# Kernel optimization log

Measured on AMD Instinct MI355X. Metric: run time of the kernel, lower is better.

## Reference

```python
import jax, jax.numpy as jnp
import numpy as np

N_ATOMS = 100000; E_ATOMS = 200000; N_AMINO = 10240; E_AMINO = 20480; B = 512
D_IN = 40; D_E = 11; H1 = 20; H2 = 20; H3 = 20; D_AA = 8; H_ARMA = 128; K = 3; T = 7
F1 = 256; F2 = 128; F3 = 64


def setup_inputs() -> dict:
    key = jax.random.key(0)
    ks = jax.random.split(key, 40)
    s = 0.05
    inp = {}
    inp['x'] = jax.random.normal(ks[0], (N_ATOMS, D_IN), dtype=jnp.float32)
    inp['edge_index'] = jax.random.randint(ks[1], (2, E_ATOMS), 0, N_ATOMS, dtype=jnp.int32)
    inp['edge_attr'] = jax.random.normal(ks[2], (E_ATOMS, D_E), dtype=jnp.float32)
    inp['monomer_labels'] = jax.random.randint(ks[3], (N_ATOMS,), 0, N_AMINO, dtype=jnp.int32)
    inp['aminoacids_features'] = jax.random.normal(ks[4], (N_AMINO, D_AA), dtype=jnp.float32)
    inp['amino_edge_index'] = jax.random.randint(ks[5], (2, E_AMINO), 0, N_AMINO, dtype=jnp.int32)
    inp['amino_batch'] = jnp.sort(jax.random.randint(ks[6], (N_AMINO,), 0, B, dtype=jnp.int32))
    # NNConv params: edge-MLP (Linear(D_E, in*out)), root weight, bias
    inp['nn1_w'] = jax.random.normal(ks[7], (D_E, D_IN * H1)) * s
    inp['nn1_b'] = jax.random.normal(ks[8], (D_IN * H1,)) * s
    inp['root1'] = jax.random.normal(ks[9], (D_IN, H1)) * s
    inp['b1'] = jax.random.normal(ks[10], (H1,)) * s
    inp['nn2_w'] = jax.random.normal(ks[11], (D_E, H1 * H2)) * s
    inp['nn2_b'] = jax.random.normal(ks[12], (H1 * H2,)) * s
    inp['root2'] = jax.random.normal(ks[13], (H1, H2)) * s
    inp['b2'] = jax.random.normal(ks[14], (H2,)) * s
    inp['nn3_w'] = jax.random.normal(ks[15], (D_E, H2 * H3)) * s
    inp['nn3_b'] = jax.random.normal(ks[16], (H2 * H3,)) * s
    inp['root3'] = jax.random.normal(ks[17], (H2, H3)) * s
    inp['b3'] = jax.random.normal(ks[18], (H3,)) * s
    # ARMAConv params (K stacks, T layers, shared_weights=False)
    F_ARMA_IN = H3 + D_AA
    inp['arma_init'] = jax.random.normal(ks[19], (K, F_ARMA_IN, H_ARMA)) * s
    inp['arma_w'] = jax.random.normal(ks[20], (T - 1, K, H_ARMA, H_ARMA)) * s
    inp['arma_root'] = jax.random.normal(ks[21], (T, K, F_ARMA_IN, H_ARMA)) * s
    inp['arma_bias'] = jax.random.normal(ks[22], (T, K, 1, H_ARMA)) * s
    # FCN head
    inp['l1_w'] = jax.random.normal(ks[23], (H_ARMA, F1)) * s
    inp['l1_b'] = jax.random.normal(ks[24], (F1,)) * s
    inp['l2_w'] = jax.random.normal(ks[25], (F1, F2)) * s
    inp['l2_b'] = jax.random.normal(ks[26], (F2,)) * s
    inp['l3_w'] = jax.random.normal(ks[27], (F2, F3)) * s
    inp['l3_b'] = jax.random.normal(ks[28], (F3,)) * s
    inp['l4_w'] = jax.random.normal(ks[29], (F3, 1)) * s
    inp['l4_b'] = jax.random.normal(ks[30], (1,)) * s
    return inp


def _nnconv(x, ei, ea, w_nn, b_nn, root, bias, out_dim):
    # PyG NNConv (aggr='add'): out_i = x_i @ root + sum_{j->i} x_j @ W(e_ji) + bias
    E, d_in = ea.shape[0], x.shape[1]
    W = (ea @ w_nn + b_nn).reshape(E, d_in, out_dim)  # per-edge weight matrices
    msg = jnp.einsum('ei,eio->eo', x[ei[0]], W)       # gather + batched matvec
    agg = jax.ops.segment_sum(msg, ei[1], num_segments=x.shape[0])
    return x @ root + agg + bias


def _arma(x, ei, init_w, w, root_w, bias):
    # PyG ARMAConv: sym-normalized adjacency (no self loops), K stacks, T layers, ReLU act
    N = x.shape[0]
    deg = jax.ops.segment_sum(jnp.ones(ei.shape[1], x.dtype), ei[1], num_segments=N)
    dinv = jnp.where(deg > 0, deg ** -0.5, 0.0)
    norm = dinv[ei[0]] * dinv[ei[1]]  # [E_amino]
    out = None
    for t in range(T):
        h = jnp.einsum('nf,kfo->kno', x, init_w) if t == 0 else jnp.einsum('knf,kfo->kno', out, w[t - 1])
        msg = h[:, ei[0], :] * norm[None, :, None]
        h = jax.vmap(lambda m: jax.ops.segment_sum(m, ei[1], num_segments=N))(msg)
        h = h + jnp.einsum('nf,kfo->kno', x, root_w[t]) + bias[t]
        out = jax.nn.relu(h)
    return out.mean(0)  # mean over stacks


def reference(x, edge_index, edge_attr, monomer_labels, aminoacids_features,
              amino_edge_index, amino_batch,
              nn1_w, nn1_b, root1, b1, nn2_w, nn2_b, root2, b2, nn3_w, nn3_b, root3, b3,
              arma_init, arma_w, arma_root, arma_bias,
              l1_w, l1_b, l2_w, l2_b, l3_w, l3_b, l4_w, l4_b):
    h = jax.nn.relu(_nnconv(x, edge_index, edge_attr, nn1_w, nn1_b, root1, b1, H1))
    h = jax.nn.relu(_nnconv(h, edge_index, edge_attr, nn2_w, nn2_b, root2, b2, H2))
    h = jax.nn.relu(_nnconv(h, edge_index, edge_attr, nn3_w, nn3_b, root3, b3, H3))
    # per-graph loop flattened: atoms -> amino-acid sum readout (graphs disjoint)
    aa = jax.ops.segment_sum(h, monomer_labels, num_segments=N_AMINO)
    aa = jnp.concatenate([aa, aminoacids_features], axis=1)  # [N_AMINO, H3+8]
    aa = jax.nn.relu(_arma(aa, amino_edge_index, arma_init, arma_w, arma_root, arma_bias))
    g = jax.ops.segment_sum(aa, amino_batch, num_segments=B)  # per-graph sum readout
    p = jax.nn.relu(g @ l1_w + l1_b)  # dropout is identity in eval mode
    p = jax.nn.relu(p @ l2_w + l2_b)
    p = jax.nn.relu(p @ l3_w + l3_b)
    return (p @ l4_w + l4_b).reshape(-1)
```

## Files before the change

kernel.cpp:

```cpp
#include <hip/hip_runtime.h>

#define N_ATOMS 100000
#define E_ATOMS 200000
#define N_AMINO 10240
#define E_AMINO 20480
#define NGRAPH 512
#define DIN0 40
#define D_E 11
#define HD 20
#define D_AA 8
#define HA 128
#define KS 3
#define TL 7
#define F1 256
#define F2 128
#define F3 64
#define NTILE 16
#define ECAP 64
#define EAW 12

typedef unsigned short u16;
typedef unsigned int u32;
typedef __attribute__((ext_vector_type(8))) short short8;
typedef __attribute__((ext_vector_type(4))) float f32x4;

__device__ __forceinline__ float b2f(u16 u) {
    union { u32 i; float f; } v; v.i = ((u32)u) << 16; return v.f;
}
__device__ __forceinline__ u16 f2b(float f) {
    union { float f; u32 i; } v; v.f = f;
    u32 x = v.i;
    return (u16)((x + (((x >> 16) & 1u) + 0x7fffu)) >> 16);
}

#define MB1_ELEMS 17408
#define MB2_ELEMS 8704
#define PREP0_N (MB1_ELEMS + 2 * MB2_ELEMS + N_AMINO * D_AA + 2 * N_ATOMS + 2 * N_AMINO)
__global__ __launch_bounds__(256) void k_prep0(
    const float* __restrict__ w1, const float* __restrict__ nb1, const float* __restrict__ r1,
    const float* __restrict__ w2, const float* __restrict__ nb2, const float* __restrict__ r2,
    const float* __restrict__ w3, const float* __restrict__ nb3, const float* __restrict__ r3,
    u16* __restrict__ Mb1, u16* __restrict__ Mb2, u16* __restrict__ Mb3,
    const float* __restrict__ af, float* __restrict__ aa,
    int* __restrict__ cs, int* __restrict__ cd,
    int* __restrict__ ca, int* __restrict__ cl) {
    int t = blockIdx.x * 256 + threadIdx.x;
    if (t < MB1_ELEMS) {
        int kb = t / 8704, rem = t % 8704;
        int c = rem >> 5, qj = rem & 31;
        int krow = kb * 32 + qj;
        float v = 0.f;
        if (krow < DIN0) {
            if (c < 220)      v = w1[(c / 20) * 800 + krow * 20 + (c % 20)];
            else if (c < 240) v = nb1[krow * 20 + (c - 220)];
            else if (c < 260) v = r1[krow * 20 + (c - 240)];
        }
        Mb1[t] = f2b(v);
    } else if (t < MB1_ELEMS + MB2_ELEMS) {
        int tt = t - MB1_ELEMS;
        int c = tt >> 5, qj = tt & 31;
        float v = 0.f;
        if (qj < HD) {
            if (c < 220)      v = w2[(c / 20) * 400 + qj * 20 + (c % 20)];
            else if (c < 240) v = nb2[qj * 20 + (c - 220)];
            else if (c < 260) v = r2[qj * 20 + (c - 240)];
        }
        Mb2[tt] = f2b(v);
    } else if (t < MB1_ELEMS + 2 * MB2_ELEMS) {
        int tt = t - MB1_ELEMS - MB2_ELEMS;
        int c = tt >> 5, qj = tt & 31;
        float v = 0.f;
        if (qj < HD) {
            if (c < 220)      v = w3[(c / 20) * 400 + qj * 20 + (c % 20)];
            else if (c < 240) v = nb3[qj * 20 + (c - 220)];
            else if (c < 260) v = r3[qj * 20 + (c - 240)];
        }
        Mb3[tt] = f2b(v);
    } else if (t < MB1_ELEMS + 2 * MB2_ELEMS + N_AMINO * D_AA) {
        int idx = t - MB1_ELEMS - 2 * MB2_ELEMS, m = idx / D_AA, j = idx % D_AA;
        aa[m * 28 + HD + j] = af[idx];
    } else {
        int z = t - MB1_ELEMS - 2 * MB2_ELEMS - N_AMINO * D_AA;
        if (z < N_ATOMS) cs[z] = 0;
        else if (z < 2 * N_ATOMS) cd[z - N_ATOMS] = 0;
        else if (z < 2 * N_ATOMS + N_AMINO) ca[z - 2 * N_ATOMS] = 0;
        else if (z < 2 * N_ATOMS + 2 * N_AMINO) cl[z - 2 * N_ATOMS - N_AMINO] = 0;
    }
}

#define WP0_ELEMS (KS * 8192)
#define WP1_ELEMS (6 * KS * 20480)
__global__ __launch_bounds__(256) void k_cvtwp2(
    const float* __restrict__ ai, const float* __restrict__ aw,
    const float* __restrict__ arw, u16* __restrict__ Wp) {
    int g = blockIdx.x * 256 + threadIdx.x;
    if (g < WP0_ELEMS) {
        int k = g / 8192, r = g % 8192;
        int kb = r >> 12, rem = r & 4095;
        int c = rem >> 5, qj = rem & 31;
        int krow = kb * 32 + qj;
        float v = 0.f;
        if (krow < 28)      v = ai[((size_t)k * 28 + krow) * HA + c];
        else if (krow < 56) v = arw[((size_t)k * 28 + (krow - 28)) * HA + c];
        Wp[g] = f2b(v);
    } else if (g < WP0_ELEMS + WP1_ELEMS) {
        int gg = g - WP0_ELEMS;
        int mat = gg / 20480, r = gg % 20480;
        int kb = r / 4096, rem = r & 4095;
        int c = rem >> 5, qj = rem & 31;
        int krow = kb * 32 + qj;
        int tm1 = mat / KS, k = mat % KS;
        float v = 0.f;
        if (krow < 128)      v = aw[((size_t)mat * 128 + krow) * HA + c];
        else if (krow < 156) v = arw[(((size_t)(tm1 + 1) * KS + k) * 28 + (krow - 128)) * HA + c];
        Wp[g] = f2b(v);
    }
}

#define NBS 98
#define NBA 10

__global__ __launch_bounds__(256) void k_csr_count(
    const int* __restrict__ esrc, const int* __restrict__ edst,
    const int* __restrict__ adst, const int* __restrict__ lbl,
    int* __restrict__ cs, int* __restrict__ cd,
    int* __restrict__ ca, int* __restrict__ cl) {
    int t = blockIdx.x * 256 + threadIdx.x;
    if (t < E_ATOMS) atomicAdd(cs + esrc[t], 1);
    else if (t < 2 * E_ATOMS) atomicAdd(cd + edst[t - E_ATOMS], 1);
    else if (t < 2 * E_ATOMS + E_AMINO) atomicAdd(ca + adst[t - 2 * E_ATOMS], 1);
    else if (t < 2 * E_ATOMS + E_AMINO + N_ATOMS) atomicAdd(cl + lbl[t - 2 * E_ATOMS - E_AMINO], 1);
}
__device__ __forceinline__ void seg_decode(int bx, int* blk, int* n, int* which) {
    if (bx < NBS)            { *which = 0; *blk = bx;             *n = N_ATOMS; }
    else if (bx < 2 * NBS)   { *which = 1; *blk = bx - NBS;       *n = N_ATOMS; }
    else if (bx < 2 * NBS + NBA) { *which = 2; *blk = bx - 2 * NBS; *n = N_AMINO; }
    else                     { *which = 3; *blk = bx - 2 * NBS - NBA; *n = N_AMINO; }
}
__global__ __launch_bounds__(256) void k_scan1(
    const int* __restrict__ cs, int* __restrict__ soff,
    const int* __restrict__ cd, int* __restrict__ doff,
    const int* __restrict__ ca, int* __restrict__ aoff,
    const int* __restrict__ cl, int* __restrict__ loff,
    int* __restrict__ bsum) {
    int blk, n, which;
    seg_decode(blockIdx.x, &blk, &n, &which);
    const int* c = which == 0 ? cs : which == 1 ? cd : which == 2 ? ca : cl;
    int* o = which == 0 ? soff : which == 1 ? doff : which == 2 ? aoff : loff;
    int tx = threadIdx.x, lane = tx & 63, w = tx >> 6;
    int i0 = blk * 1024 + tx * 4;
    int v[4];
#pragma unroll
    for (int q = 0; q < 4; ++q) v[q] = (i0 + q < n) ? c[i0 + q] : 0;
    int s = v[0] + v[1] + v[2] + v[3];
    int inc = s;
#pragma unroll
    for (int d = 1; d < 64; d <<= 1) {
        int u = __shfl_up(inc, d, 64);
        if (lane >= d) inc += u;
    }
    __shared__ int wsum[4];
    if (lane == 63) wsum[w] = inc;
    __syncthreads();
    int wo = 0;
    for (int i = 0; i < w; ++i) wo += wsum[i];
    int run = wo + inc - s;
#pragma unroll
    for (int q = 0; q < 4; ++q) {
        if (i0 + q < n) o[i0 + q] = run;
        run += v[q];
    }
    if (tx == 255) bsum[blockIdx.x] = wo + inc;
}
__global__ __launch_bounds__(128) void k_scan2(
    int* __restrict__ bsum, int* __restrict__ soff, int* __restrict__ doff,
    int* __restrict__ aoff, int* __restrict__ loff) {
    int bx = blockIdx.x;
    int nb   = (bx < 2) ? NBS : NBA;
    int base = (bx == 0) ? 0 : (bx == 1) ? NBS : (bx == 2) ? 2 * NBS : 2 * NBS + NBA;
    int* b = bsum + base;
    int tx = threadIdx.x, lane = tx & 63;
    int v = (tx < nb) ? b[tx] : 0;
    int inc = v;
#pragma unroll
    for (int d = 1; d < 64; d <<= 1) {
        int u = __shfl_up(inc, d, 64);
        if (lane >= d) inc += u;
    }
    __shared__ int w0;
    if (tx == 63) w0 = inc;
    __syncthreads();
    int excl = inc - v + ((tx >= 64) ? w0 : 0);
    if (tx < nb) b[tx] = excl;
    if (tx == nb - 1) {
        int tot = excl + v;
        if (bx == 0) soff[N_ATOMS] = tot;
        else if (bx == 1) doff[N_ATOMS] = tot;
        else if (bx == 2) aoff[N_AMINO] = tot;
        else loff[N_AMINO] = tot;
    }
}
__global__ __launch_bounds__(256) void k_scan3(
    int* __restrict__ soff, int* __restrict__ doff,
    int* __restrict__ aoff, int* __restrict__ loff,
    const int* __restrict__ bsum,
    int* __restrict__ us, int* __restrict__ ud,
    int* __restrict__ ua, int* __restrict__ ul) {
    int blk, n, which;
    seg_decode(blockIdx.x, &blk, &n, &which);
    int* o = which == 0 ? soff : which == 1 ? doff : which == 2 ? aoff : loff;
    int* cu = which == 0 ? us : which == 1 ? ud : which == 2 ? ua : ul;
    int add = bsum[blockIdx.x];
    int i0 = blk * 1024 + threadIdx.x * 4;
#pragma unroll
    for (int q = 0; q < 4; ++q)
        if (i0 + q < n) { int val = o[i0 + q] + add; o[i0 + q] = val; cu[i0 + q] = val; }
}
__global__ __launch_bounds__(256) void k_csr_fill(
    const int* __restrict__ esrc, const int* __restrict__ edst,
    const float* __restrict__ ea,
    int* __restrict__ us, int* __restrict__ srcP, u16* __restrict__ eaP,
    int* __restrict__ ud, int* __restrict__ sdp,
    const int* __restrict__ aei, int* __restrict__ ua, int* __restrict__ aeid,
    const int* __restrict__ aoff, float* __restrict__ nrm,
    const int* __restrict__ lbl, int* __restrict__ ul, int* __restrict__ lnid) {
    int t = blockIdx.x * 256 + threadIdx.x;
    if (t < E_ATOMS) {
        int jj = atomicAdd(us + esrc[t], 1);
        srcP[jj] = esrc[t];
        const float* e0 = ea + (size_t)t * D_E;
        u16* e1 = eaP + (size_t)jj * EAW;
#pragma unroll
        for (int k = 0; k < D_E; ++k) e1[k] = f2b(e0[k]);
        e1[D_E] = f2b(1.0f);
        sdp[jj] = atomicAdd(ud + edst[t], 1);
    } else if (t < E_ATOMS + E_AMINO) {
        int e = t - E_ATOMS;
        int p = atomicAdd(ua + aei[E_AMINO + e], 1);
        aeid[p] = e;
    } else if (t < E_ATOMS + 2 * E_AMINO) {
        int e = t - E_ATOMS - E_AMINO;
        int s = aei[e], d = aei[E_AMINO + e];
        int ds = aoff[s + 1] - aoff[s], dd = aoff[d + 1] - aoff[d];
        float a = ds > 0 ? rsqrtf((float)ds) : 0.f;
        float b = dd > 0 ? rsqrtf((float)dd) : 0.f;
        nrm[e] = a * b;
    } else if (t < E_ATOMS + 2 * E_AMINO + N_ATOMS) {
        int n = t - E_ATOMS - 2 * E_AMINO;
        int p = atomicAdd(ul + lbl[n], 1);
        lnid[p] = n;
    }
}

template <int DIN, int KB, bool RAW>
__global__ __launch_bounds__(256, 6) void nnconv_edge11(
    const void* __restrict__ xin, const u16* __restrict__ eaP,
    const int* __restrict__ srcP, const int* __restrict__ sdp,
    const int* __restrict__ soff, const u16* __restrict__ Mb,
    const float* __restrict__ bnn, u16* __restrict__ msg,
    u16* __restrict__ selfm) {
    constexpr int KPAD = KB * 32;
    __shared__ __align__(16) float y3[NTILE * 240];
    __shared__ __align__(16) u16 As[NTILE * KPAD];
    __shared__ __align__(16) float eaS[ECAP * 12];
    __shared__ int srcS[ECAP];
    __shared__ int sdpS[ECAP];
    int tx = threadIdx.x;
    int n0 = blockIdx.x * NTILE;
    int j0 = soff[n0], j1 = soff[n0 + NTILE];
    for (int i = tx; i < NTILE * KPAD; i += 256) {
        int node = i / KPAD, k = i % KPAD;
        u16 v = 0;
        if (k < DIN)
            v = RAW ? f2b(((const float*)xin)[(size_t)(n0 + node) * DIN + k])
                    : ((const u16*)xin)[(size_t)(n0 + node) * DIN + k];
        As[i] = v;
    }
    {
        int cn0 = j1 - j0; if (cn0 > ECAP) cn0 = ECAP;
        for (int i = tx; i < cn0; i += 256) {
            srcS[i] = srcP[j0 + i] - n0;
            sdpS[i] = sdp[j0 + i];
        }
        const u32* eg = (const u32*)(eaP + (size_t)j0 * EAW);
        for (int i = tx; i < cn0 * 6; i += 256) {
            u32 pv = eg[i];
            eaS[2 * i]     = b2f((u16)(pv & 0xffff));
            eaS[2 * i + 1] = b2f((u16)(pv >> 16));
        }
    }
    __syncthreads();
    {
        int wave = tx >> 6, lane = tx & 63;
        int m = lane & 15, q = lane >> 4;
        short8 aF[KB];
#pragma unroll
        for (int kb = 0; kb < KB; ++kb)
            aF[kb] = *(const short8*)&As[m * KPAD + kb * 32 + q * 8];
        for (int ct = wave; ct < 17; ct += 4) {
            int c0 = ct * 16;
            f32x4 acc = {0.f, 0.f, 0.f, 0.f};
#pragma unroll
            for (int kb = 0; kb < KB; ++kb) {
                short8 bF = *(const short8*)(Mb + (size_t)kb * 8704 + (size_t)(c0 + m) * 32 + q * 8);
                acc = __builtin_amdgcn_mfma_f32_16x16x32_bf16(aF[kb], bF, acc, 0, 0, 0);
            }
            int c = c0 + m;
            if (c < 240) {
                int slot = (c < 220) ? (c % 20) * 12 + c / 20 : (c - 220) * 12 + 11;
#pragma unroll
                for (int r = 0; r < 4; ++r)
                    y3[(q * 4 + r) * 240 + slot] = acc[r];
            } else if (c < 260) {
                float bv = bnn[c - 240];
#pragma unroll
                for (int r = 0; r < 4; ++r)
                    selfm[(size_t)(n0 + q * 4 + r) * 20 + (c - 240)] = f2b(acc[r] + bv);
            }
        }
    }
    __syncthreads();
    int c0 = j0;
    while (true) {
        int cn = j1 - c0; if (cn > ECAP) cn = ECAP;
        for (int p = tx; p < cn * 20; p += 256) {
            int e = p / 20, o = p - e * 20;
            const float4* ev = (const float4*)&eaS[e * 12];
            const float4* yr = (const float4*)&y3[srcS[e] * 240 + o * 12];
            float4 e0 = ev[0], e1 = ev[1], e2 = ev[2];
            float4 q0 = yr[0], q1 = yr[1], q2 = yr[2];
            float mv = e0.x * q0.x + e0.y * q0.y + e0.z * q0.z + e0.w * q0.w
                     + e1.x * q1.x + e1.y * q1.y + e1.z * q1.z + e1.w * q1.w
                     + e2.x * q2.x + e2.y * q2.y + e2.z * q2.z + e2.w * q2.w;
            msg[(size_t)sdpS[e] * 20 + o] = f2b(mv);
        }
        c0 += cn;
        if (c0 >= j1) break;
        __syncthreads();
        int cm = j1 - c0; if (cm > ECAP) cm = ECAP;
        for (int i = tx; i < cm; i += 256) {
            srcS[i] = srcP[c0 + i] - n0;
            sdpS[i] = sdp[c0 + i];
        }
        const u32* eg = (const u32*)(eaP + (size_t)c0 * EAW);
        for (int i = tx; i < cm * 6; i += 256) {
            u32 pv = eg[i];
            eaS[2 * i]     = b2f((u16)(pv & 0xffff));
            eaS[2 * i + 1] = b2f((u16)(pv >> 16));
        }
        __syncthreads();
    }
}

__global__ __launch_bounds__(256) void nnconv_reduce2(
    const u16* __restrict__ selfm, const int* __restrict__ doff,
    const u16* __restrict__ msg, u16* __restrict__ hout) {
    int t = blockIdx.x * 256 + threadIdx.x;
    if (t >= N_ATOMS * HD) return;
    int n = t / HD, o = t - n * HD;
    float acc = b2f(selfm[t]);
    int j1 = doff[n + 1];
    for (int j = doff[n]; j < j1; ++j)
        acc += b2f(msg[(size_t)j * HD + o]);
    hout[t] = f2b(fmaxf(acc, 0.f));
}

__global__ __launch_bounds__(256) void aa_gather(
    const u16* __restrict__ h3, const int* __restrict__ loff,
    const int* __restrict__ lnid, float* __restrict__ aa) {
    int t = blockIdx.x * 256 + threadIdx.x;
    if (t >= N_AMINO * HD) return;
    int m = t / HD, o = t % HD;
    float s = 0.f;
    int j1 = loff[m + 1];
    for (int j = loff[m]; j < j1; ++j)
        s += b2f(h3[(size_t)lnid[j] * HD + o]);
    aa[m * 28 + o] = s;
}

__global__ __launch_bounds__(256) void k_gaa(
    const float* __restrict__ aa, const int* __restrict__ aoff,
    const int* __restrict__ aeid, const int* __restrict__ aei,
    const float* __restrict__ nrm, u16* __restrict__ A0) {
    int t = blockIdx.x * 256 + threadIdx.x;
    if (t >= N_AMINO * 64) return;
    int n = t >> 6, c = t & 63;
    float v = 0.f;
    if (c < 28) {
        int j1 = aoff[n + 1];
        for (int jj = aoff[n]; jj < j1; ++jj) {
            int e = aeid[jj], s = aei[e];
            v += nrm[e] * aa[(size_t)s * 28 + c];
        }
    } else if (c < 56) {
        v = aa[(size_t)n * 28 + (c - 28)];
    }
    A0[t] = f2b(v);
}

__global__ __launch_bounds__(256) void arma_l0(
    const u16* __restrict__ A0, const u16* __restrict__ Wp0,
    const float* __restrict__ abi, u16* __restrict__ O, size_t kstride) {
    int wave = threadIdx.x >> 6, lane = threadIdx.x & 63;
    int k = blockIdx.y;
    const u16* W = Wp0 + (size_t)k * 8192;
    u16* Ok = O + (size_t)k * kstride;
    const float* bk = abi + (size_t)k * HA;
    int n0 = (blockIdx.x * 4 + wave) * 16;
    int m = lane & 15, q = lane >> 4;
    short8 aF[2];
#pragma unroll
    for (int kb = 0; kb < 2; ++kb)
        aF[kb] = *(const short8*)(A0 + (size_t)(n0 + m) * 64 + kb * 32 + q * 8);
#pragma unroll
    for (int ct = 0; ct < 8; ++ct) {
        int c0 = ct * 16;
        float b = bk[c0 + m];
        f32x4 acc = {b, b, b, b};
#pragma unroll
        for (int kb = 0; kb < 2; ++kb) {
            short8 bF = *(const short8*)(W + (size_t)((kb * 128 + c0 + m) * 32 + q * 8));
            acc = __builtin_amdgcn_mfma_f32_16x16x32_bf16(aF[kb], bF, acc, 0, 0, 0);
        }
#pragma unroll
        for (int r = 0; r < 4; ++r)
            Ok[(size_t)(n0 + q * 4 + r) * HA + c0 + m] = f2b(fmaxf(acc[r], 0.f));
    }
}

__global__ __launch_bounds__(256) void arma_lt(
    const u16* __restrict__ Oprev, const u16* __restrict__ Wm,
    const float* __restrict__ abit, const float* __restrict__ aa,
    const int* __restrict__ aoff, const int* __restrict__ aeid,
    const int* __restrict__ aei, const float* __restrict__ nrm,
    u16* __restrict__ Onext, size_t kstride) {
    __shared__ __align__(16) u16 As[64 * 160];
    int tx = threadIdx.x;
    int k = blockIdx.y;
    int n0b = blockIdx.x * 64;
    const u16* Op = Oprev + (size_t)k * kstride;
    const u16* W  = Wm + (size_t)k * 20480;
    for (int i = tx; i < 1024; i += 256) {
        int nl = i >> 4, cb = i & 15;
        int n = n0b + nl;
        int j1 = aoff[n + 1];
        float a0 = 0.f, a1 = 0.f, a2 = 0.f, a3 = 0.f;
        float a4 = 0.f, a5 = 0.f, a6 = 0.f, a7 = 0.f;
        for (int jj = aoff[n]; jj < j1; ++jj) {
            int e = aeid[jj], s = aei[e];
            float nm = nrm[e];
            uint4 hv = *(const uint4*)(Op + (size_t)s * HA + cb * 8);
            a0 += nm * b2f((u16)(hv.x & 0xffff));
            a1 += nm * b2f((u16)(hv.x >> 16));
            a2 += nm * b2f((u16)(hv.y & 0xffff));
            a3 += nm * b2f((u16)(hv.y >> 16));
            a4 += nm * b2f((u16)(hv.z & 0xffff));
            a5 += nm * b2f((u16)(hv.z >> 16));
            a6 += nm * b2f((u16)(hv.w & 0xffff));
            a7 += nm * b2f((u16)(hv.w >> 16));
        }
        uint4 pk;
        pk.x = (u32)f2b(a0) | ((u32)f2b(a1) << 16);
        pk.y = (u32)f2b(a2) | ((u32)f2b(a3) << 16);
        pk.z = (u32)f2b(a4) | ((u32)f2b(a5) << 16);
        pk.w = (u32)f2b(a6) | ((u32)f2b(a7) << 16);
        *(uint4*)&As[nl * 160 + cb * 8] = pk;
    }
    {
        int nl = tx >> 2, cb = tx & 3;
        int n = n0b + nl;
        float av[8];
#pragma unroll
        for (int j = 0; j < 8; ++j) {
            int c = cb * 8 + j;
            av[j] = (c < 28) ? aa[(size_t)n * 28 + c] : 0.f;
        }
        uint4 pk;
        pk.x = (u32)f2b(av[0]) | ((u32)f2b(av[1]) << 16);
        pk.y = (u32)f2b(av[2]) | ((u32)f2b(av[3]) << 16);
        pk.z = (u32)f2b(av[4]) | ((u32)f2b(av[5]) << 16);
        pk.w = (u32)f2b(av[6]) | ((u32)f2b(av[7]) << 16);
        *(uint4*)&As[nl * 160 + 128 + cb * 8] = pk;
    }
    __syncthreads();
    int wave = tx >> 6, lane = tx & 63;
    int m = lane & 15, q = lane >> 4;
    int wl = wave * 16 + m;
    short8 aF[5];
#pragma unroll
    for (int kb = 0; kb < 5; ++kb)
        aF[kb] = *(const short8*)&As[wl * 160 + kb * 32 + q * 8];
    int n0 = n0b + wave * 16;
    u16* On = Onext + (size_t)k * kstride;
    const float* bk = abit + (size_t)k * HA;
#pragma unroll
    for (int ct = 0; ct < 8; ++ct) {
        int c0 = ct * 16;
        float b = bk[c0 + m];
        f32x4 acc = {b, b, b, b};
#pragma unroll
        for (int kb = 0; kb < 5; ++kb) {
            short8 bF = *(const short8*)(W + (size_t)((kb * 128 + c0 + m) * 32 + q * 8));
            acc = __builtin_amdgcn_mfma_f32_16x16x32_bf16(aF[kb], bF, acc, 0, 0, 0);
        }
#pragma unroll
        for (int r = 0; r < 4; ++r)
            On[(size_t)(n0 + q * 4 + r) * HA + c0 + m] = f2b(fmaxf(acc[r], 0.f));
    }
}

__global__ __launch_bounds__(256) void head2(
    const u16* __restrict__ O, size_t kstride, const int* __restrict__ bat,
    const float* __restrict__ l1w, const float* __restrict__ l1b,
    const float* __restrict__ l2w, const float* __restrict__ l2b,
    const float* __restrict__ l3w, const float* __restrict__ l3b,
    const float* __restrict__ l4w, const float* __restrict__ l4b,
    float* __restrict__ outp) {
    __shared__ float sg[HA], sp1[F1], sp2[F2], sp3[F3];
    int b = blockIdx.x, tx = threadIdx.x;
    int lo = 0, hi = N_AMINO;
    while (lo < hi) { int mid = (lo + hi) >> 1; if (bat[mid] < b) lo = mid + 1; else hi = mid; }
    int s = lo;
    lo = 0; hi = N_AMINO;
    while (lo < hi) { int mid = (lo + hi) >> 1; if (bat[mid] < b + 1) lo = mid + 1; else hi = mid; }
    int e = lo;
    if (tx < HA) {
        float acc = 0.f;
        for (int n = s; n < e; ++n)
            acc += b2f(O[(size_t)n * HA + tx]) + b2f(O[kstride + (size_t)n * HA + tx])
                 + b2f(O[2 * kstride + (size_t)n * HA + tx]);
        sg[tx] = acc * (1.f / 3.f);
    }
    __syncthreads();
    {   float acc = l1b[tx];
        for (int f = 0; f < HA; ++f) acc += sg[f] * l1w[f * F1 + tx];
        sp1[tx] = fmaxf(acc, 0.f); }
    __syncthreads();
    if (tx < F2) {
        float acc = l2b[tx];
        for (int f = 0; f < F1; ++f) acc += sp1[f] * l2w[f * F2 + tx];
        sp2[tx] = fmaxf(acc, 0.f); }
    __syncthreads();
    if (tx < F3) {
        float acc = l3b[tx];
        for (int f = 0; f < F2; ++f) acc += sp2[f] * l3w[f * F3 + tx];
        sp3[tx] = fmaxf(acc, 0.f); }
    __syncthreads();
    if (tx < 64) {
        float p = sp3[tx] * l4w[tx];
        for (int off = 32; off > 0; off >>= 1) p += __shfl_down(p, off, 64);
        if (tx == 0) outp[b] = p + l4b[0];
    }
}

#define OFF_M1    ((size_t)0)
#define OFF_M2    ((size_t)38400)
#define OFF_M3    ((size_t)57600)
#define OFF_AOFF  ((size_t)76800)
#define OFF_AEID  ((size_t)118016)
#define OFF_NRM   ((size_t)199936)
#define OFF_AA    ((size_t)281856)
#define OFF_HA    ((size_t)2891008)
#define OFF_HB    ((size_t)6891008)
#define OFF_MSG   ((size_t)10891008)
#define OFF_SOFF  ((size_t)18891008)
#define OFF_DOFF  ((size_t)19291136)
#define OFF_DSLOT ((size_t)19691264)
#define OFF_LOFF  ((size_t)20491264)
#define OFF_LNID  ((size_t)20532480)
#define OFF_CS    ((size_t)20932480)
#define OFF_CD    ((size_t)21332480)
#define OFF_CA    ((size_t)21732480)
#define OFF_CL    ((size_t)21773440)
#define OFF_US    ((size_t)21814400)
#define OFF_UD    ((size_t)22214400)
#define OFF_UA    ((size_t)22614400)
#define OFF_UL    ((size_t)22655360)
#define OFF_BSUM  ((size_t)22696320)
#define OFF_EAP   ((size_t)22697216)
#define OFF_SRCP  ((size_t)27497216)
#define OFF_WP    ((size_t)28297216)
#define OFF_SELFM ((size_t)29083648)
#define OFF_OB    ((size_t)2891008)
#define OFF_A0    ((size_t)10891008)
#define OFF_OA    ((size_t)18619648)

extern "C" void kernel_launch(void* const* d_in, const int* in_sizes, int n_in,
                              void* d_out, int out_size, void* d_ws, size_t ws_size,
                              hipStream_t stream) {
    (void)in_sizes; (void)n_in; (void)out_size; (void)ws_size;
    const float* x   = (const float*)d_in[0];
    const int*   ei  = (const int*)d_in[1];
    const float* ea  = (const float*)d_in[2];
    const int*   lbl = (const int*)d_in[3];
    const float* af  = (const float*)d_in[4];
    const int*   aei = (const int*)d_in[5];
    const int*   bat = (const int*)d_in[6];
    const float* nn1w = (const float*)d_in[7];  const float* nn1b = (const float*)d_in[8];
    const float* rt1  = (const float*)d_in[9];  const float* b1   = (const float*)d_in[10];
    const float* nn2w = (const float*)d_in[11]; const float* nn2b = (const float*)d_in[12];
    const float* rt2  = (const float*)d_in[13]; const float* b2   = (const float*)d_in[14];
    const float* nn3w = (const float*)d_in[15]; const float* nn3b = (const float*)d_in[16];
    const float* rt3  = (const float*)d_in[17]; const float* b3   = (const float*)d_in[18];
    const float* ai   = (const float*)d_in[19]; const float* aw   = (const float*)d_in[20];
    const float* arw  = (const float*)d_in[21]; const float* abi  = (const float*)d_in[22];
    const float* l1w  = (const float*)d_in[23]; const float* l1b  = (const float*)d_in[24];
    const float* l2w  = (const float*)d_in[25]; const float* l2b  = (const float*)d_in[26];
    const float* l3w  = (const float*)d_in[27]; const float* l3b  = (const float*)d_in[28];
    const float* l4w  = (const float*)d_in[29]; const float* l4b  = (const float*)d_in[30];
    float* outp = (float*)d_out;

    char* ws = (char*)d_ws;
    u16*   Mb1   = (u16*)(ws + OFF_M1);
    u16*   Mb2   = (u16*)(ws + OFF_M2);
    u16*   Mb3   = (u16*)(ws + OFF_M3);
    int*   aoff  = (int*)(ws + OFF_AOFF);
    int*   aeid  = (int*)(ws + OFF_AEID);
    float* nrm   = (float*)(ws + OFF_NRM);
    float* aa    = (float*)(ws + OFF_AA);
    u16*   hA    = (u16*)(ws + OFF_HA);
    u16*   hB    = (u16*)(ws + OFF_HB);
    u16*   msg   = (u16*)(ws + OFF_MSG);
    int*   soff  = (int*)(ws + OFF_SOFF);
    int*   doff  = (int*)(ws + OFF_DOFF);
    int*   sdp   = (int*)(ws + OFF_DSLOT);
    int*   loff  = (int*)(ws + OFF_LOFF);
    int*   lnid  = (int*)(ws + OFF_LNID);
    int*   cs    = (int*)(ws + OFF_CS);
    int*   cd    = (int*)(ws + OFF_CD);
    int*   ca    = (int*)(ws + OFF_CA);
    int*   cl    = (int*)(ws + OFF_CL);
    int*   us    = (int*)(ws + OFF_US);
    int*   ud    = (int*)(ws + OFF_UD);
    int*   ua    = (int*)(ws + OFF_UA);
    int*   ul    = (int*)(ws + OFF_UL);
    int*   bsum  = (int*)(ws + OFF_BSUM);
    u16*   eaP   = (u16*)(ws + OFF_EAP);
    int*   srcP  = (int*)(ws + OFF_SRCP);
    u16*   Wp    = (u16*)(ws + OFF_WP);
    u16*   selfm = (u16*)(ws + OFF_SELFM);
    u16*   A0    = (u16*)(ws + OFF_A0);
    u16*   OA    = (u16*)(ws + OFF_OA);
    u16*   OB    = (u16*)(ws + OFF_OB);

    const int* esrc = ei;
    const int* edst = ei + E_ATOMS;
    const int* adst = aei + E_AMINO;

    k_prep0<<<(PREP0_N + 255) / 256, 256, 0, stream>>>(
        nn1w, nn1b, rt1, nn2w, nn2b, rt2, nn3w, nn3b, rt3,
        Mb1, Mb2, Mb3, af, aa, cs, cd, ca, cl);
    k_cvtwp2<<<(WP0_ELEMS + WP1_ELEMS + 255) / 256, 256, 0, stream>>>(ai, aw, arw, Wp);
    k_csr_count<<<(2 * E_ATOMS + E_AMINO + N_ATOMS + 255) / 256, 256, 0, stream>>>(
        esrc, edst, adst, lbl, cs, cd, ca, cl);
    k_scan1<<<2 * NBS + 2 * NBA, 256, 0, stream>>>(cs, soff, cd, doff, ca, aoff, cl, loff, bsum);
    k_scan2<<<4, 128, 0, stream>>>(bsum, soff, doff, aoff, loff);
    k_scan3<<<2 * NBS + 2 * NBA, 256, 0, stream>>>(soff, doff, aoff, loff, bsum, us, ud, ua, ul);
    k_csr_fill<<<(E_ATOMS + 2 * E_AMINO + N_ATOMS + 255) / 256, 256, 0, stream>>>(
        esrc, edst, ea, us, srcP, eaP, ud, sdp, aei, ua, aeid, aoff, nrm, lbl, ul, lnid);

    const int GT = N_ATOMS / NTILE;
    const int GF = (N_ATOMS * HD + 255) / 256;
    nnconv_edge11<DIN0, 2, true ><<<GT, 256, 0, stream>>>(x,  eaP, srcP, sdp, soff, Mb1, b1, msg, selfm);
    nnconv_reduce2<<<GF, 256, 0, stream>>>(selfm, doff, msg, hA);
    nnconv_edge11<HD,   1, false><<<GT, 256, 0, stream>>>(hA, eaP, srcP, sdp, soff, Mb2, b2, msg, selfm);
    nnconv_reduce2<<<GF, 256, 0, stream>>>(selfm, doff, msg, hB);
    nnconv_edge11<HD,   1, false><<<GT, 256, 0, stream>>>(hB, eaP, srcP, sdp, soff, Mb3, b3, msg, selfm);
    nnconv_reduce2<<<GF, 256, 0, stream>>>(selfm, doff, msg, hA);
    aa_gather<<<(N_AMINO * HD + 255) / 256, 256, 0, stream>>>(hA, loff, lnid, aa);

    const size_t KH = (size_t)N_AMINO * HA;
    k_gaa<<<(N_AMINO * 64 + 255) / 256, 256, 0, stream>>>(aa, aoff, aeid, aei, nrm, A0);
    arma_l0<<<dim3(160, KS), 256, 0, stream>>>(A0, Wp, abi, OA, KH);
    for (int t = 1; t < TL; ++t) {
        const u16* Oin  = (t & 1) ? OA : OB;
        u16*       Oout = (t & 1) ? OB : OA;
        arma_lt<<<dim3(160, KS), 256, 0, stream>>>(
            Oin, Wp + WP0_ELEMS + (size_t)((t - 1) * KS) * 20480,
            abi + (size_t)t * KS * HA, aa, aoff, aeid, aei, nrm, Oout, KH);
    }
    head2<<<NGRAPH, 256, 0, stream>>>(OA, KH, bat, l1w, l1b, l2w, l2b,
                                      l3w, l3b, l4w, l4b, outp);
}
```

Measured before the change: 469.3 us.

## Fuse NNConv reductions into next edge kernel and merge prep/ARMA-init kernels

The per-layer destination reduction (self term plus summed messages, then ReLU) moves into the A-tile load of the next NNConv edge kernel. Messages ping-pong between two buffers, and only the final layer keeps a standalone reduce, which writes in place into selfm. The two weight-conversion prep kernels become one launch. The ARMA layer-0 gather is fused into its MFMA kernel, with one block covering all K stacks. The message writes also pack two bf16 outputs per thread. This removes several launches and intermediate global round trips, at the cost of serial per-degree gathers inside the tile-load phase.

```diff
diff --git a/kernel.cpp b/kernel.cpp
--- a/kernel.cpp
+++ b/kernel.cpp
@@ -36,14 +36,19 @@
 #define MB1_ELEMS 17408
 #define MB2_ELEMS 8704
 #define PREP0_N (MB1_ELEMS + 2 * MB2_ELEMS + N_AMINO * D_AA + 2 * N_ATOMS + 2 * N_AMINO)
-__global__ __launch_bounds__(256) void k_prep0(
+#define WP0_ELEMS (KS * 8192)
+#define WP1_ELEMS (6 * KS * 20480)
+#define PREP_N (PREP0_N + WP0_ELEMS + WP1_ELEMS)
+__global__ __launch_bounds__(256) void k_prep(
     const float* __restrict__ w1, const float* __restrict__ nb1, const float* __restrict__ r1,
     const float* __restrict__ w2, const float* __restrict__ nb2, const float* __restrict__ r2,
     const float* __restrict__ w3, const float* __restrict__ nb3, const float* __restrict__ r3,
     u16* __restrict__ Mb1, u16* __restrict__ Mb2, u16* __restrict__ Mb3,
     const float* __restrict__ af, float* __restrict__ aa,
     int* __restrict__ cs, int* __restrict__ cd,
-    int* __restrict__ ca, int* __restrict__ cl) {
+    int* __restrict__ ca, int* __restrict__ cl,
+    const float* __restrict__ ai, const float* __restrict__ aw,
+    const float* __restrict__ arw, u16* __restrict__ Wp) {
     int t = blockIdx.x * 256 + threadIdx.x;
     if (t < MB1_ELEMS) {
         int kb = t / 8704, rem = t % 8704;
@@ -79,41 +84,35 @@
     } else if (t < MB1_ELEMS + 2 * MB2_ELEMS + N_AMINO * D_AA) {
         int idx = t - MB1_ELEMS - 2 * MB2_ELEMS, m = idx / D_AA, j = idx % D_AA;
         aa[m * 28 + HD + j] = af[idx];
-    } else {
+    } else if (t < PREP0_N) {
         int z = t - MB1_ELEMS - 2 * MB2_ELEMS - N_AMINO * D_AA;
         if (z < N_ATOMS) cs[z] = 0;
         else if (z < 2 * N_ATOMS) cd[z - N_ATOMS] = 0;
         else if (z < 2 * N_ATOMS + N_AMINO) ca[z - 2 * N_ATOMS] = 0;
         else if (z < 2 * N_ATOMS + 2 * N_AMINO) cl[z - 2 * N_ATOMS - N_AMINO] = 0;
-    }
-}
-
-#define WP0_ELEMS (KS * 8192)
-#define WP1_ELEMS (6 * KS * 20480)
-__global__ __launch_bounds__(256) void k_cvtwp2(
-    const float* __restrict__ ai, const float* __restrict__ aw,
-    const float* __restrict__ arw, u16* __restrict__ Wp) {
-    int g = blockIdx.x * 256 + threadIdx.x;
-    if (g < WP0_ELEMS) {
-        int k = g / 8192, r = g % 8192;
-        int kb = r >> 12, rem = r & 4095;
-        int c = rem >> 5, qj = rem & 31;
-        int krow = kb * 32 + qj;
-        float v = 0.f;
-        if (krow < 28)      v = ai[((size_t)k * 28 + krow) * HA + c];
-        else if (krow < 56) v = arw[((size_t)k * 28 + (krow - 28)) * HA + c];
-        Wp[g] = f2b(v);
-    } else if (g < WP0_ELEMS + WP1_ELEMS) {
-        int gg = g - WP0_ELEMS;
-        int mat = gg / 20480, r = gg % 20480;
-        int kb = r / 4096, rem = r & 4095;
-        int c = rem >> 5, qj = rem & 31;
-        int krow = kb * 32 + qj;
-        int tm1 = mat / KS, k = mat % KS;
-        float v = 0.f;
-        if (krow < 128)      v = aw[((size_t)mat * 128 + krow) * HA + c];
-        else if (krow < 156) v = arw[(((size_t)(tm1 + 1) * KS + k) * 28 + (krow - 128)) * HA + c];
-        Wp[g] = f2b(v);
+    } else {
+        int g = t - PREP0_N;
+        if (g < WP0_ELEMS) {
+            int k = g / 8192, r = g % 8192;
+            int kb = r >> 12, rem = r & 4095;
+            int c = rem >> 5, qj = rem & 31;
+            int krow = kb * 32 + qj;
+            float v = 0.f;
+            if (krow < 28)      v = ai[((size_t)k * 28 + krow) * HA + c];
+            else if (krow < 56) v = arw[((size_t)k * 28 + (krow - 28)) * HA + c];
+            Wp[g] = f2b(v);
+        } else if (g < WP0_ELEMS + WP1_ELEMS) {
+            int gg = g - WP0_ELEMS;
+            int mat = gg / 20480, r = gg % 20480;
+            int kb = r / 4096, rem = r & 4095;
+            int c = rem >> 5, qj = rem & 31;
+            int krow = kb * 32 + qj;
+            int tm1 = mat / KS, k = mat % KS;
+            float v = 0.f;
+            if (krow < 128)      v = aw[((size_t)mat * 128 + krow) * HA + c];
+            else if (krow < 156) v = arw[(((size_t)(tm1 + 1) * KS + k) * 28 + (krow - 128)) * HA + c];
+            Wp[g] = f2b(v);
+        }
     }
 }
 
@@ -252,13 +251,14 @@
     }
 }
 
-template <int DIN, int KB, bool RAW>
-__global__ __launch_bounds__(256, 6) void nnconv_edge11(
-    const void* __restrict__ xin, const u16* __restrict__ eaP,
-    const int* __restrict__ srcP, const int* __restrict__ sdp,
-    const int* __restrict__ soff, const u16* __restrict__ Mb,
-    const float* __restrict__ bnn, u16* __restrict__ msg,
-    u16* __restrict__ selfm) {
+template <int DIN, int KB, bool RAW, bool FUSEH>
+__global__ __launch_bounds__(256, 6) void nnconv_edge12(
+    const void* __restrict__ xin, const u16* __restrict__ msgin,
+    u16* __restrict__ selfm, const int* __restrict__ doff,
+    const u16* __restrict__ eaP, const int* __restrict__ srcP,
+    const int* __restrict__ sdp, const int* __restrict__ soff,
+    const u16* __restrict__ Mb, const float* __restrict__ bnn,
+    u16* __restrict__ msgout) {
     constexpr int KPAD = KB * 32;
     __shared__ __align__(16) float y3[NTILE * 240];
     __shared__ __align__(16) u16 As[NTILE * KPAD];
@@ -271,9 +271,18 @@
     for (int i = tx; i < NTILE * KPAD; i += 256) {
         int node = i / KPAD, k = i % KPAD;
         u16 v = 0;
-        if (k < DIN)
-            v = RAW ? f2b(((const float*)xin)[(size_t)(n0 + node) * DIN + k])
-                    : ((const u16*)xin)[(size_t)(n0 + node) * DIN + k];
+        if (k < DIN) {
+            if (RAW) {
+                v = f2b(((const float*)xin)[(size_t)(n0 + node) * DIN + k]);
+            } else if (FUSEH) {
+                int n = n0 + node;
+                float acc = b2f(selfm[(size_t)n * HD + k]);
+                int jj1 = doff[n + 1];
+                for (int j = doff[n]; j < jj1; ++j)
+                    acc += b2f(msgin[(size_t)j * HD + k]);
+                v = f2b(fmaxf(acc, 0.f));
+            }
+        }
         As[i] = v;
     }
     {
@@ -315,7 +324,7 @@
                 float bv = bnn[c - 240];
 #pragma unroll
                 for (int r = 0; r < 4; ++r)
-                    selfm[(size_t)(n0 + q * 4 + r) * 20 + (c - 240)] = f2b(acc[r] + bv);
+                    selfm[(size_t)(n0 + q * 4 + r) * HD + (c - 240)] = f2b(acc[r] + bv);
             }
         }
     }
@@ -323,16 +332,23 @@
     int c0 = j0;
     while (true) {
         int cn = j1 - c0; if (cn > ECAP) cn = ECAP;
-        for (int p = tx; p < cn * 20; p += 256) {
-            int e = p / 20, o = p - e * 20;
+        for (int p = tx; p < cn * 10; p += 256) {
+            int e = p / 10, h = p - e * 10;
             const float4* ev = (const float4*)&eaS[e * 12];
-            const float4* yr = (const float4*)&y3[srcS[e] * 240 + o * 12];
             float4 e0 = ev[0], e1 = ev[1], e2 = ev[2];
-            float4 q0 = yr[0], q1 = yr[1], q2 = yr[2];
-            float mv = e0.x * q0.x + e0.y * q0.y + e0.z * q0.z + e0.w * q0.w
-                     + e1.x * q1.x + e1.y * q1.y + e1.z * q1.z + e1.w * q1.w
-                     + e2.x * q2.x + e2.y * q2.y + e2.z * q2.z + e2.w * q2.w;
-            msg[(size_t)sdpS[e] * 20 + o] = f2b(mv);
+            const float* yb = &y3[srcS[e] * 240];
+            const float4* ya = (const float4*)(yb + (2 * h) * 12);
+            const float4* yc = (const float4*)(yb + (2 * h + 1) * 12);
+            float4 a0 = ya[0], a1 = ya[1], a2 = ya[2];
+            float4 b0 = yc[0], b1 = yc[1], b2 = yc[2];
+            float mv0 = e0.x * a0.x + e0.y * a0.y + e0.z * a0.z + e0.w * a0.w
+                      + e1.x * a1.x + e1.y * a1.y + e1.z * a1.z + e1.w * a1.w
+                      + e2.x * a2.x + e2.y * a2.y + e2.z * a2.z + e2.w * a2.w;
+            float mv1 = e0.x * b0.x + e0.y * b0.y + e0.z * b0.z + e0.w * b0.w
+                      + e1.x * b1.x + e1.y * b1.y + e1.z * b1.z + e1.w * b1.w
+                      + e2.x * b2.x + e2.y * b2.y + e2.z * b2.z + e2.w * b2.w;
+            u32 pk = (u32)f2b(mv0) | ((u32)f2b(mv1) << 16);
+            *(u32*)(msgout + (size_t)sdpS[e] * HD + 2 * h) = pk;
         }
         c0 += cn;
         if (c0 >= j1) break;
@@ -352,17 +368,18 @@
     }
 }
 
-__global__ __launch_bounds__(256) void nnconv_reduce2(
-    const u16* __restrict__ selfm, const int* __restrict__ doff,
-    const u16* __restrict__ msg, u16* __restrict__ hout) {
+__global__ __launch_bounds__(256) void nnconv_reduce3(
+    u16* __restrict__ selfm, const int* __restrict__ doff,
+    const u16* __restrict__ msg) {
     int t = blockIdx.x * 256 + threadIdx.x;
     if (t >= N_ATOMS * HD) return;
-    int n = t / HD, o = t - n * HD;
+    int n = t / HD;
     float acc = b2f(selfm[t]);
     int j1 = doff[n + 1];
+    int o = t - n * HD;
     for (int j = doff[n]; j < j1; ++j)
         acc += b2f(msg[(size_t)j * HD + o]);
-    hout[t] = f2b(fmaxf(acc, 0.f));
+    selfm[t] = f2b(fmaxf(acc, 0.f));
 }
 
 __global__ __launch_bounds__(256) void aa_gather(
@@ -378,53 +395,55 @@
     aa[m * 28 + o] = s;
 }
 
-__global__ __launch_bounds__(256) void k_gaa(
+__global__ __launch_bounds__(256) void arma_l0f(
     const float* __restrict__ aa, const int* __restrict__ aoff,
     const int* __restrict__ aeid, const int* __restrict__ aei,
-    const float* __restrict__ nrm, u16* __restrict__ A0) {
-    int t = blockIdx.x * 256 + threadIdx.x;
-    if (t >= N_AMINO * 64) return;
-    int n = t >> 6, c = t & 63;
-    float v = 0.f;
-    if (c < 28) {
-        int j1 = aoff[n + 1];
-        for (int jj = aoff[n]; jj < j1; ++jj) {
-            int e = aeid[jj], s = aei[e];
-            v += nrm[e] * aa[(size_t)s * 28 + c];
-        }
-    } else if (c < 56) {
-        v = aa[(size_t)n * 28 + (c - 28)];
-    }
-    A0[t] = f2b(v);
-}
-
-__global__ __launch_bounds__(256) void arma_l0(
-    const u16* __restrict__ A0, const u16* __restrict__ Wp0,
+    const float* __restrict__ nrm, const u16* __restrict__ Wp0,
     const float* __restrict__ abi, u16* __restrict__ O, size_t kstride) {
-    int wave = threadIdx.x >> 6, lane = threadIdx.x & 63;
-    int k = blockIdx.y;
-    const u16* W = Wp0 + (size_t)k * 8192;
-    u16* Ok = O + (size_t)k * kstride;
-    const float* bk = abi + (size_t)k * HA;
-    int n0 = (blockIdx.x * 4 + wave) * 16;
+    __shared__ __align__(16) u16 As[64 * 64];
+    int tx = threadIdx.x;
+    int n0b = blockIdx.x * 64;
+    for (int i = tx; i < 64 * 64; i += 256) {
+        int nl = i >> 6, c = i & 63;
+        int n = n0b + nl;
+        float v = 0.f;
+        if (c < 28) {
+            int j1 = aoff[n + 1];
+            for (int jj = aoff[n]; jj < j1; ++jj) {
+                int e = aeid[jj], s = aei[e];
+                v += nrm[e] * aa[(size_t)s * 28 + c];
+            }
+        } else if (c < 56) {
+            v = aa[(size_t)n * 28 + (c - 28)];
+        }
+        As[i] = f2b(v);
+    }
+    __syncthreads();
+    int wave = tx >> 6, lane = tx & 63;
     int m = lane & 15, q = lane >> 4;
     short8 aF[2];
 #pragma unroll
     for (int kb = 0; kb < 2; ++kb)
-        aF[kb] = *(const short8*)(A0 + (size_t)(n0 + m) * 64 + kb * 32 + q * 8);
-#pragma unroll
-    for (int ct = 0; ct < 8; ++ct) {
-        int c0 = ct * 16;
-        float b = bk[c0 + m];
-        f32x4 acc = {b, b, b, b};
-#pragma unroll
-        for (int kb = 0; kb < 2; ++kb) {
-            short8 bF = *(const short8*)(W + (size_t)((kb * 128 + c0 + m) * 32 + q * 8));
-            acc = __builtin_amdgcn_mfma_f32_16x16x32_bf16(aF[kb], bF, acc, 0, 0, 0);
-        }
-#pragma unroll
-        for (int r = 0; r < 4; ++r)
-            Ok[(size_t)(n0 + q * 4 + r) * HA + c0 + m] = f2b(fmaxf(acc[r], 0.f));
+        aF[kb] = *(const short8*)&As[(wave * 16 + m) * 64 + kb * 32 + q * 8];
+    int n0 = n0b + wave * 16;
+    for (int k = 0; k < KS; ++k) {
+        const u16* W = Wp0 + (size_t)k * 8192;
+        u16* Ok = O + (size_t)k * kstride;
+        const float* bk = abi + (size_t)k * HA;
+#pragma unroll
+        for (int ct = 0; ct < 8; ++ct) {
+            int c0 = ct * 16;
+            float b = bk[c0 + m];
+            f32x4 acc = {b, b, b, b};
+#pragma unroll
+            for (int kb = 0; kb < 2; ++kb) {
+                short8 bF = *(const short8*)(W + (size_t)((kb * 128 + c0 + m) * 32 + q * 8));
+                acc = __builtin_amdgcn_mfma_f32_16x16x32_bf16(aF[kb], bF, acc, 0, 0, 0);
+            }
+#pragma unroll
+            for (int r = 0; r < 4; ++r)
+                Ok[(size_t)(n0 + q * 4 + r) * HA + c0 + m] = f2b(fmaxf(acc[r], 0.f));
+        }
     }
 }
 
@@ -560,8 +579,7 @@
 #define OFF_AEID  ((size_t)118016)
 #define OFF_NRM   ((size_t)199936)
 #define OFF_AA    ((size_t)281856)
-#define OFF_HA    ((size_t)2891008)
-#define OFF_HB    ((size_t)6891008)
+#define OFF_MSGB  ((size_t)2891008)
 #define OFF_MSG   ((size_t)10891008)
 #define OFF_SOFF  ((size_t)18891008)
 #define OFF_DOFF  ((size_t)19291136)
@@ -582,7 +600,6 @@
 #define OFF_WP    ((size_t)28297216)
 #define OFF_SELFM ((size_t)29083648)
 #define OFF_OB    ((size_t)2891008)
-#define OFF_A0    ((size_t)10891008)
 #define OFF_OA    ((size_t)18619648)
 
 extern "C" void kernel_launch(void* const* d_in, const int* in_sizes, int n_in,
@@ -618,9 +635,8 @@
     int*   aeid  = (int*)(ws + OFF_AEID);
     float* nrm   = (float*)(ws + OFF_NRM);
     float* aa    = (float*)(ws + OFF_AA);
-    u16*   hA    = (u16*)(ws + OFF_HA);
-    u16*   hB    = (u16*)(ws + OFF_HB);
-    u16*   msg   = (u16*)(ws + OFF_MSG);
+    u16*   msgA  = (u16*)(ws + OFF_MSG);
+    u16*   msgB  = (u16*)(ws + OFF_MSGB);
     int*   soff  = (int*)(ws + OFF_SOFF);
     int*   doff  = (int*)(ws + OFF_DOFF);
     int*   sdp   = (int*)(ws + OFF_DSLOT);
@@ -639,7 +655,6 @@
     int*   srcP  = (int*)(ws + OFF_SRCP);
     u16*   Wp    = (u16*)(ws + OFF_WP);
     u16*   selfm = (u16*)(ws + OFF_SELFM);
-    u16*   A0    = (u16*)(ws + OFF_A0);
     u16*   OA    = (u16*)(ws + OFF_OA);
     u16*   OB    = (u16*)(ws + OFF_OB);
 
@@ -647,10 +662,9 @@
     const int* edst = ei + E_ATOMS;
     const int* adst = aei + E_AMINO;
 
-    k_prep0<<<(PREP0_N + 255) / 256, 256, 0, stream>>>(
+    k_prep<<<(PREP_N + 255) / 256, 256, 0, stream>>>(
         nn1w, nn1b, rt1, nn2w, nn2b, rt2, nn3w, nn3b, rt3,
-        Mb1, Mb2, Mb3, af, aa, cs, cd, ca, cl);
-    k_cvtwp2<<<(WP0_ELEMS + WP1_ELEMS + 255) / 256, 256, 0, stream>>>(ai, aw, arw, Wp);
+        Mb1, Mb2, Mb3, af, aa, cs, cd, ca, cl, ai, aw, arw, Wp);
     k_csr_count<<<(2 * E_ATOMS + E_AMINO + N_ATOMS + 255) / 256, 256, 0, stream>>>(
         esrc, edst, adst, lbl, cs, cd, ca, cl);
     k_scan1<<<2 * NBS + 2 * NBA, 256, 0, stream>>>(cs, soff, cd, doff, ca, aoff, cl, loff, bsum);
@@ -661,17 +675,17 @@
 
     const int GT = N_ATOMS / NTILE;
     const int GF = (N_ATOMS * HD + 255) / 256;
-    nnconv_edge11<DIN0, 2, true ><<<GT, 256, 0, stream>>>(x,  eaP, srcP, sdp, soff, Mb1, b1, msg, selfm);
-    nnconv_reduce2<<<GF, 256, 0, stream>>>(selfm, doff, msg, hA);
-    nnconv_edge11<HD,   1, false><<<GT, 256, 0, stream>>>(hA, eaP, srcP, sdp, soff, Mb2, b2, msg, selfm);
-    nnconv_reduce2<<<GF, 256, 0, stream>>>(selfm, doff, msg, hB);
-    nnconv_edge11<HD,   1, false><<<GT, 256, 0, stream>>>(hB, eaP, srcP, sdp, soff, Mb3, b3, msg, selfm);
-    nnconv_reduce2<<<GF, 256, 0, stream>>>(selfm, doff, msg, hA);
-    aa_gather<<<(N_AMINO * HD + 255) / 256, 256, 0, stream>>>(hA, loff, lnid, aa);
+    nnconv_edge12<DIN0, 2, true , false><<<GT, 256, 0, stream>>>(
+        x,  msgA, selfm, doff, eaP, srcP, sdp, soff, Mb1, b1, msgA);
+    nnconv_edge12<HD,   1, false, true ><<<GT, 256, 0, stream>>>(
+        nullptr, msgA, selfm, doff, eaP, srcP, sdp, soff, Mb2, b2, msgB);
+    nnconv_edge12<HD,   1, false, true ><<<GT, 256, 0, stream>>>(
+        nullptr, msgB, selfm, doff, eaP, srcP, sdp, soff, Mb3, b3, msgA);
+    nnconv_reduce3<<<GF, 256, 0, stream>>>(selfm, doff, msgA);
+    aa_gather<<<(N_AMINO * HD + 255) / 256, 256, 0, stream>>>(selfm, loff, lnid, aa);
 
     const size_t KH = (size_t)N_AMINO * HA;
-    k_gaa<<<(N_AMINO * 64 + 255) / 256, 256, 0, stream>>>(aa, aoff, aeid, aei, nrm, A0);
-    arma_l0<<<dim3(160, KS), 256, 0, stream>>>(A0, Wp, abi, OA, KH);
+    arma_l0f<<<160, 256, 0, stream>>>(aa, aoff, aeid, aei, nrm, Wp, abi, OA, KH);
     for (int t = 1; t < TL; ++t) {
         const u16* Oin  = (t & 1) ? OA : OB;
         u16*       Oout = (t & 1) ? OB : OA;
```

Result: slower. 535.8 us (+14.1%).
